# Performance work log

Measured on AMD Instinct MI355X. Metric: run time of the kernel, lower is better.

## Reference

```python
import jax, jax.numpy as jnp
import numpy as np

# Kornia's fixed 5x5 pyramid (binomial) kernel used by build_pyramid/pyrdown
_PYR_K = np.array([[1, 4, 6, 4, 1],
                   [4, 16, 24, 16, 4],
                   [6, 24, 36, 24, 6],
                   [4, 16, 24, 16, 4],
                   [1, 4, 6, 4, 1]], dtype=np.float32) / 256.0


def _pyrdown(x):
    """kornia pyrdown: 5x5 binomial blur (reflect pad) + bilinear resize to (H//2, W//2)."""
    B, C, H, W = x.shape
    xp = jnp.pad(x, ((0, 0), (0, 0), (2, 2), (2, 2)), mode='reflect')
    k = jnp.broadcast_to(jnp.asarray(_PYR_K, x.dtype), (C, 1, 5, 5))  # depthwise
    y = jax.lax.conv_general_dilated(
        xp, k, window_strides=(1, 1), padding='VALID',
        feature_group_count=C, dimension_numbers=('NCHW', 'OIHW', 'NCHW'))
    # torch F.interpolate bilinear align_corners=False == jax resize bilinear, antialias off
    return jax.image.resize(y, (B, C, H // 2, W // 2), method='bilinear', antialias=False)


def _norm_pc(x):
    """Per-channel min-max normalization to [0,1] over spatial dims."""
    mx = jnp.max(x, axis=(2, 3), keepdims=True)
    mn = jnp.min(x, axis=(2, 3), keepdims=True)
    return (x - mn) / (mx - mn)


def _avg_local_max(x):
    """Mean of 16x16 tile maxima; torch loop range(0, H-16, 16) skips the last tile
    row/col, and with zero tiles the torch code yields nan_to_num(0/0) == 0."""
    B, C, H, W = x.shape
    s = 16
    ny = len(range(0, H - s, s))
    nx = len(range(0, W - s, s))
    if ny == 0 or nx == 0:
        return jnp.zeros((B, C, 1, 1), x.dtype)
    t = x[:, :, :ny * s, :nx * s].reshape(B, C, ny, s, nx, s)
    lmax = jnp.max(t, axis=(3, 5))           # [B,C,ny,nx]
    return jnp.mean(lmax, axis=(2, 3)).reshape(B, C, 1, 1)


def _sm_normalization(x):
    d = _norm_pc(x)
    lm = _avg_local_max(d)
    return d * (1.0 - lm) ** 2


def setup_inputs() -> dict:
    key = jax.random.key(0)
    x = jax.random.normal(key, (8, 3, 512, 512), dtype=jnp.float32)
    return {"x": x}


def reference(x):
    B, C, H, W = x.shape
    inp = _norm_pc(x)
    max_level = int(H).bit_length() - 1   # 9 for H=512
    u = max_level - 1

    # Gaussian pyramid of length max_level: [inp, pyrdown(inp), ...]
    pyr = [inp]
    for _ in range(max_level - 1):
        pyr.append(_pyrdown(pyr[-1]))

    acc = None
    for i in range(u - 1):
        h, w = pyr[i + 1].shape[2], pyr[i + 1].shape[3]
        up = jnp.repeat(jnp.repeat(pyr[i + 2], 2, axis=2), 2, axis=3)[:, :, :h, :w]
        d = jnp.abs(pyr[i + 1] - up)
        nd = jax.image.resize(_sm_normalization(d), (B, C, H, W),
                              method='bilinear', antialias=False)
        acc = nd if acc is None else acc + nd

    return jnp.mean(acc, axis=1)  # [B,H,W]
```

## Files before the change

### kernel.cpp

```cpp
#include <hip/hip_runtime.h>
#include <math.h>

#define NPLANES 24
#define BLK 256
#define FINF 3.402823466e38f

__host__ __device__ __forceinline__ int d_off(int li) {
    return 2097152 - (2097152 >> (2 * li));
}

__device__ __forceinline__ int refl(int v, int S) {
    if (v < 0) v = -v;
    if (v >= S) v = 2 * S - 2 - v;
    return v;
}

__device__ __forceinline__ float bredMin(float v, float* red, int tid) {
    red[tid] = v; __syncthreads();
    for (int s = 128; s > 0; s >>= 1) {
        if (tid < s) red[tid] = fminf(red[tid], red[tid + s]);
        __syncthreads();
    }
    float r = red[0]; __syncthreads(); return r;
}
__device__ __forceinline__ float bredMax(float v, float* red, int tid) {
    red[tid] = v; __syncthreads();
    for (int s = 128; s > 0; s >>= 1) {
        if (tid < s) red[tid] = fmaxf(red[tid], red[tid + s]);
        __syncthreads();
    }
    float r = red[0]; __syncthreads(); return r;
}
__device__ __forceinline__ float bredSum(float v, float* red, int tid) {
    red[tid] = v; __syncthreads();
    for (int s = 128; s > 0; s >>= 1) {
        if (tid < s) red[tid] += red[tid + s];
        __syncthreads();
    }
    float r = red[0]; __syncthreads(); return r;
}

__device__ __forceinline__ float stencil6(const float* s, int S, int i, int j) {
    const float w[6] = {1.f, 5.f, 10.f, 10.f, 5.f, 1.f};
    int rx[6];
#pragma unroll
    for (int b = 0; b < 6; ++b) rx[b] = refl(2 * j - 2 + b, S);
    float acc = 0.f;
#pragma unroll
    for (int a = 0; a < 6; ++a) {
        int ry = refl(2 * i - 2 + a, S);
        const float* rp = s + ry * S;
        float r = 0.f;
#pragma unroll
        for (int b = 0; b < 6; ++b) r += w[b] * rp[rx[b]];
        acc += w[a] * r;
    }
    return acc * (1.f / 1024.f);
}

template <int IS, bool HAS_D, int LI>
__global__ __launch_bounds__(256) void pyrdown_tiled(const float* __restrict__ in,
                                                     float* __restrict__ out,
                                                     float* __restrict__ dout,
                                                     float* __restrict__ tileMin,
                                                     float* __restrict__ tileMax) {
    constexpr int SO = IS / 2;
    constexpr int TO = 32;
    constexpr int TI = 2 * TO + 4;
    constexpr int TPA = SO / TO;
    __shared__ float sIn[TI * TI];
    __shared__ float sH[TI * TO];
    __shared__ float sOut[TO * TO];
    __shared__ float sD[HAS_D ? 64 * 65 : 1];
    __shared__ float rmn[HAS_D ? 256 : 1], rmx[HAS_D ? 256 : 1];

    const int tid = threadIdx.x;
    const int p = blockIdx.x / (TPA * TPA);
    const int t = blockIdx.x % (TPA * TPA);
    const int ty = t / TPA, tx = t % TPA;
    const int oy = ty * TO, ox = tx * TO;
    const int iy = 2 * oy - 2, ix = 2 * ox - 2;
    const float* ip = in + (size_t)p * IS * IS;

    for (int k = tid; k < TI * TI; k += 256) {
        int r = k / TI, c = k - r * TI;
        sIn[k] = ip[refl(iy + r, IS) * IS + refl(ix + c, IS)];
    }
    __syncthreads();

    for (int k = tid; k < TI * TO; k += 256) {
        int r = k / TO, j = k - r * TO;
        const float* rp = sIn + r * TI + 2 * j;
        sH[k] = rp[0] + 5.f * rp[1] + 10.f * rp[2] + 10.f * rp[3] + 5.f * rp[4] + rp[5];
    }
    __syncthreads();

    float* op = out + (size_t)p * SO * SO;
    for (int k = tid; k < TO * TO; k += 256) {
        int i = k / TO, j = k - i * TO;
        const float* cp = sH + (2 * i) * TO + j;
        float v = (cp[0] + 5.f * cp[TO] + 10.f * cp[2 * TO] + 10.f * cp[3 * TO] +
                   5.f * cp[4 * TO] + cp[5 * TO]) * (1.f / 1024.f);
        sOut[k] = v;
        op[(size_t)(oy + i) * SO + ox + j] = v;
    }

    if (HAS_D) {
        __syncthreads();
        float* dp = dout + (size_t)p * IS * IS;
        for (int k = tid; k < 4096; k += 256) {
            int yy = k >> 6, xx = k & 63;
            float dv = fabsf(sIn[(yy + 2) * TI + xx + 2] - sOut[(yy >> 1) * TO + (xx >> 1)]);
            sD[yy * 65 + xx] = dv;
            dp[(size_t)(2 * oy + yy) * IS + 2 * ox + xx] = dv;
        }
        __syncthreads();
        int s = tid >> 4, r = tid & 15;
        int tr = s >> 2, tc = s & 3;
        const float* rowp = sD + (tr * 16 + r) * 65 + tc * 16;
        float mn = FINF, mx = -FINF;
#pragma unroll
        for (int c = 0; c < 16; ++c) {
            float v = rowp[c];
            mn = fminf(mn, v); mx = fmaxf(mx, v);
        }
        rmn[tid] = mn; rmx[tid] = mx;
        __syncthreads();
        for (int st = 8; st > 0; st >>= 1) {
            if (r < st) {
                rmn[tid] = fminf(rmn[tid], rmn[tid + st]);
                rmx[tid] = fmaxf(rmx[tid], rmx[tid + st]);
            }
            __syncthreads();
        }
        if (r == 0) {
            constexpr int TA = IS / 16;
            constexpr int baseLi = (LI == 0) ? 0 : 6144;
            int gidx = baseLi + p * TA * TA + (ty * 4 + tr) * TA + (tx * 4 + tc);
            tileMin[gidx] = rmn[tid];
            tileMax[gidx] = rmx[tid];
        }
    }
}

__global__ __launch_bounds__(256) void fused_small_kernel(const float* __restrict__ pyr3,
                                                          float* __restrict__ dBase,
                                                          float* __restrict__ A,
                                                          float* __restrict__ B) {
    __shared__ float sp3[4096], sd2[4096];
    __shared__ float sp4[1024], sd3[1024];
    __shared__ float sp5[256], sd4[256];
    __shared__ float sp6[64], sd5[64];
    __shared__ float sp7[16], sd6[16];
    __shared__ float red[256];
    __shared__ float tmaxLds[16];
    const int tid = threadIdx.x;
    const int p = blockIdx.x;
    const float* g3 = pyr3 + (size_t)p * 4096;
    for (int k = tid; k < 4096; k += 256) sp3[k] = g3[k];
    __syncthreads();

    float* d2g = dBase + d_off(2) + (size_t)p * 4096;
    for (int k = tid; k < 1024; k += 256) {
        int i = k >> 5, j = k & 31;
        float v = stencil6(sp3, 64, i, j);
        sp4[k] = v;
#pragma unroll
        for (int di = 0; di < 2; ++di)
#pragma unroll
            for (int dj = 0; dj < 2; ++dj) {
                int y = 2 * i + di, x = 2 * j + dj;
                float dv = fabsf(sp3[y * 64 + x] - v);
                sd2[y * 64 + x] = dv;
                d2g[y * 64 + x] = dv;
            }
    }
    __syncthreads();

    {
        int i = tid >> 4, j = tid & 15;
        float v = stencil6(sp4, 32, i, j);
        sp5[tid] = v;
        float* d3g = dBase + d_off(3) + (size_t)p * 1024;
#pragma unroll
        for (int di = 0; di < 2; ++di)
#pragma unroll
            for (int dj = 0; dj < 2; ++dj) {
                int y = 2 * i + di, x = 2 * j + dj;
                float dv = fabsf(sp4[y * 32 + x] - v);
                sd3[y * 32 + x] = dv;
                d3g[y * 32 + x] = dv;
            }
    }
    __syncthreads();

    if (tid < 64) {
        int i = tid >> 3, j = tid & 7;
        float v = stencil6(sp5, 16, i, j);
        sp6[tid] = v;
        float* d4g = dBase + d_off(4) + (size_t)p * 256;
#pragma unroll
        for (int di = 0; di < 2; ++di)
#pragma unroll
            for (int dj = 0; dj < 2; ++dj) {
                int y = 2 * i + di, x = 2 * j + dj;
                float dv = fabsf(sp5[y * 16 + x] - v);
                sd4[y * 16 + x] = dv;
                d4g[y * 16 + x] = dv;
            }
    }
    __syncthreads();

    if (tid < 16) {
        int i = tid >> 2, j = tid & 3;
        float v = stencil6(sp6, 8, i, j);
        sp7[tid] = v;
        float* d5g = dBase + d_off(5) + (size_t)p * 64;
#pragma unroll
        for (int di = 0; di < 2; ++di)
#pragma unroll
            for (int dj = 0; dj < 2; ++dj) {
                int y = 2 * i + di, x = 2 * j + dj;
                float dv = fabsf(sp6[y * 8 + x] - v);
                sd5[y * 8 + x] = dv;
                d5g[y * 8 + x] = dv;
            }
    }
    __syncthreads();

    if (tid < 4) {
        int i = tid >> 1, j = tid & 1;
        float v = stencil6(sp7, 4, i, j);
        float* d6g = dBase + d_off(6) + (size_t)p * 16;
#pragma unroll
        for (int di = 0; di < 2; ++di)
#pragma unroll
            for (int dj = 0; dj < 2; ++dj) {
                int y = 2 * i + di, x = 2 * j + dj;
                float dv = fabsf(sp7[y * 4 + x] - v);
                sd6[y * 4 + x] = dv;
                d6g[y * 4 + x] = dv;
            }
    }
    __syncthreads();

    {
        float mn = FINF, mx = -FINF;
        for (int k = tid; k < 4096; k += 256) {
            float v = sd2[k];
            mn = fminf(mn, v); mx = fmaxf(mx, v);
        }
        mn = bredMin(mn, red, tid);
        mx = bredMax(mx, red, tid);
        {
            int t = tid >> 4, r = tid & 15;
            int ty = t >> 2, tx = t & 3;
            const float* rowp = sd2 + (ty * 16 + r) * 64 + tx * 16;
            float sm = -FINF;
#pragma unroll
            for (int c = 0; c < 16; ++c) sm = fmaxf(sm, rowp[c]);
            red[tid] = sm;
        }
        __syncthreads();
        if (tid < 16) {
            float tm = -FINF;
            for (int r = 0; r < 16; ++r) tm = fmaxf(tm, red[tid * 16 + r]);
            tmaxLds[tid] = tm;
        }
        __syncthreads();
        if (tid == 0) {
            float s = 0.f;
            for (int ty = 0; ty < 3; ++ty)
                for (int tx = 0; tx < 3; ++tx) s += tmaxLds[ty * 4 + tx];
            float inv = 1.f / (mx - mn);
            float lm = (s * (1.f / 9.f) - mn) * inv;
            float g = (1.f - lm) * (1.f - lm);
            A[2 * NPLANES + p] = g * inv;
            B[2 * NPLANES + p] = -mn * g * inv;
        }
        __syncthreads();
    }
    {
        float mn = FINF, mx = -FINF;
        for (int k = tid; k < 1024; k += 256) {
            float v = sd3[k];
            mn = fminf(mn, v); mx = fmaxf(mx, v);
        }
        mn = bredMin(mn, red, tid);
        mx = bredMax(mx, red, tid);
        float e = sd3[(tid >> 4) * 32 + (tid & 15)];
        float tm = bredMax(e, red, tid);
        if (tid == 0) {
            float inv = 1.f / (mx - mn);
            float lm = (tm - mn) * inv;
            float g = (1.f - lm) * (1.f - lm);
            A[3 * NPLANES + p] = g * inv;
            B[3 * NPLANES + p] = -mn * g * inv;
        }
    }
    {
        float v = sd4[tid];
        float mn = bredMin(v, red, tid);
        float mx = bredMax(v, red, tid);
        if (tid == 0) {
            float inv = 1.f / (mx - mn);
            A[4 * NPLANES + p] = inv; B[4 * NPLANES + p] = -mn * inv;
        }
    }
    {
        float v = (tid < 64) ? sd5[tid] : FINF;
        float mn = bredMin(v, red, tid);
        v = (tid < 64) ? sd5[tid] : -FINF;
        float mx = bredMax(v, red, tid);
        if (tid == 0) {
            float inv = 1.f / (mx - mn);
            A[5 * NPLANES + p] = inv; B[5 * NPLANES + p] = -mn * inv;
        }
    }
    {
        float v = (tid < 16) ? sd6[tid] : FINF;
        float mn = bredMin(v, red, tid);
        v = (tid < 16) ? sd6[tid] : -FINF;
        float mx = bredMax(v, red, tid);
        if (tid == 0) {
            float inv = 1.f / (mx - mn);
            A[6 * NPLANES + p] = inv; B[6 * NPLANES + p] = -mn * inv;
        }
    }
}

__global__ __launch_bounds__(256) void reduce_kernel(const float* __restrict__ tileMin,
                                                     const float* __restrict__ tileMax,
                                                     float* __restrict__ A,
                                                     float* __restrict__ B) {
    __shared__ float red[256];
    int li = blockIdx.x / NPLANES;
    int p = blockIdx.x % NPLANES;
    int tid = threadIdx.x;
    int TP = (li == 0) ? 256 : 64;
    int TA = (li == 0) ? 16 : 8;
    int nt = TA - 1;
    int base = (li == 0) ? p * 256 : 6144 + p * 64;
    float tmn = (tid < TP) ? tileMin[base + tid] : FINF;
    float tmx = (tid < TP) ? tileMax[base + tid] : -FINF;
    float mn = bredMin(tmn, red, tid);
    float mx = bredMax(tmx, red, tid);
    int ty = (li == 0) ? (tid >> 4) : (tid >> 3);
    int tx = (li == 0) ? (tid & 15) : (tid & 7);
    float s = (tid < TP && ty < nt && tx < nt) ? tmx : 0.f;
    float sum = bredSum(s, red, tid);
    if (tid == 0) {
        float ntiles = (float)(nt * nt);
        float inv = 1.f / (mx - mn);
        float lm = (sum / ntiles - mn) * inv;
        float g = (1.f - lm) * (1.f - lm);
        A[li * NPLANES + p] = g * inv;
        B[li * NPLANES + p] = -mn * g * inv;
    }
}

__global__ __launch_bounds__(256) void final_kernel(const float* __restrict__ dBase,
                                                    const float* __restrict__ A,
                                                    const float* __restrict__ Bc,
                                                    float* __restrict__ out) {
    __shared__ float patch[1650];
    __shared__ float sBtot;
    const int tid = threadIdx.x;
    const int b = blockIdx.x >> 6;
    const int tile = blockIdx.x & 63;
    const int yb = (tile >> 3) << 6;
    const int xb = (tile & 7) << 6;

    if (tid == 0) {
        float s = 0.f;
        for (int k = 0; k < 7; ++k)
            for (int c = 0; c < 3; ++c) s += Bc[k * NPLANES + b * 3 + c];
        sBtot = s;
    }

    const int dims[7] = {34, 18, 10, 6, 4, 3, 3};
    const int lofs[7] = {0, 1156, 1480, 1580, 1616, 1632, 1641};
    int baseY[7], baseX[7];
#pragma unroll
    for (int li = 0; li < 7; ++li) {
        const int S = 256 >> li;
        const float s = 1.f / (float)(2 << li);
        baseY[li] = (int)floorf((yb + 0.5f) * s - 0.5f);
        baseX[li] = (int)floorf((xb + 0.5f) * s - 0.5f);
        const int dim = dims[li];
        const int n = dim * dim;
        const float* d0p = dBase + d_off(li) + (size_t)(b * 3) * S * S;
        const float* d1p = d0p + S * S;
        const float* d2p = d1p + S * S;
        const float A0 = A[li * NPLANES + b * 3 + 0];
        const float A1 = A[li * NPLANES + b * 3 + 1];
        const float A2 = A[li * NPLANES + b * 3 + 2];
        for (int k = tid; k < n; k += 256) {
            int r = k / dim, c = k - r * dim;
            int sr = min(max(baseY[li] + r, 0), S - 1);
            int sc = min(max(baseX[li] + c, 0), S - 1);
            int si = sr * S + sc;
            patch[lofs[li] + k] = A0 * d0p[si] + A1 * d1p[si] + A2 * d2p[si];
        }
    }
    __syncthreads();

    const int ty = tid >> 4, tx = tid & 15;
    const int gy0 = yb + (ty << 2), gx0 = xb + (tx << 2);
    float acc[4][4];
#pragma unroll
    for (int i = 0; i < 4; ++i)
#pragma unroll
        for (int j = 0; j < 4; ++j) acc[i][j] = 0.f;

#pragma unroll
    for (int li = 0; li < 7; ++li) {
        const int dim = dims[li];
        const float* P = patch + lofs[li];
        const float s = 1.f / (float)(2 << li);
        int pr[4], pc[4];
        float wy[4], wx[4];
#pragma unroll
        for (int k = 0; k < 4; ++k) {
            float fy = (gy0 + k + 0.5f) * s - 0.5f;
            float fl = floorf(fy);
            wy[k] = fy - fl;
            pr[k] = (int)fl - baseY[li];
            float fx = (gx0 + k + 0.5f) * s - 0.5f;
            fl = floorf(fx);
            wx[k] = fx - fl;
            pc[k] = (int)fl - baseX[li];
        }
#pragma unroll
        for (int i = 0; i < 4; ++i) {
            const float* r0 = P + pr[i] * dim;
            const float* r1 = r0 + dim;
#pragma unroll
            for (int j = 0; j < 4; ++j) {
                float a0 = r0[pc[j]], a1 = r0[pc[j] + 1];
                float b0 = r1[pc[j]], b1 = r1[pc[j] + 1];
                float h0 = a0 + wx[j] * (a1 - a0);
                float h1 = b0 + wx[j] * (b1 - b0);
                acc[i][j] += h0 + wy[i] * (h1 - h0);
            }
        }
    }

    const float bt = sBtot;
    float* op = out + ((size_t)b * 512 + gy0) * 512 + gx0;
#pragma unroll
    for (int i = 0; i < 4; ++i) {
        float4 v;
        v.x = (acc[i][0] + bt) * (1.f / 3.f);
        v.y = (acc[i][1] + bt) * (1.f / 3.f);
        v.z = (acc[i][2] + bt) * (1.f / 3.f);
        v.w = (acc[i][3] + bt) * (1.f / 3.f);
        *(float4*)(op + (size_t)i * 512) = v;
    }
}

extern "C" void kernel_launch(void* const* d_in, const int* in_sizes, int n_in,
                              void* d_out, int out_size, void* d_ws, size_t ws_size,
                              hipStream_t stream) {
    (void)in_sizes; (void)n_in; (void)out_size; (void)ws_size;
    const float* x = (const float*)d_in[0];
    float* ws = (float*)d_ws;
    float* out = (float*)d_out;

    float* pyr1 = ws;
    float* pyr2 = ws + 1572864;
    float* pyr3 = ws + 1966080;
    float* dBase = ws + 2064384;
    float* tileMin = ws + 4161408;
    float* tileMax = ws + 4169088;
    float* A = ws + 4176768;
    float* Bc = ws + 4176936;

    pyrdown_tiled<512, false, 0><<<NPLANES * 64, 256, 0, stream>>>(x, pyr1, nullptr, nullptr, nullptr);
    pyrdown_tiled<256, true, 0><<<NPLANES * 16, 256, 0, stream>>>(pyr1, pyr2, dBase + d_off(0), tileMin, tileMax);
    pyrdown_tiled<128, true, 1><<<NPLANES * 4, 256, 0, stream>>>(pyr2, pyr3, dBase + d_off(1), tileMin, tileMax);
    fused_small_kernel<<<NPLANES, 256, 0, stream>>>(pyr3, dBase, A, Bc);
    reduce_kernel<<<2 * NPLANES, 256, 0, stream>>>(tileMin, tileMax, A, Bc);
    final_kernel<<<8 * 64, 256, 0, stream>>>(dBase, A, Bc, out);
}
```

Before: 126.3 us.

## Fuse pyramid levels into two kernels and drop separate reduce pass

Merges the first two pyrdown levels into one tiled kernel that computes level 1 in shared memory with halo and writes only level-2 output plus d0 and tile min/max. Folds the level-2→3 pyrdown, the level-1 difference stats, and the former reduce_kernel into a per-plane monolithic kernel alongside the small-level chain. This removes the pyr1/pyr3 global round trips and three launches. In exchange it adds redundant halo recompute in the fused kernel and puts more serial work on only 24 blocks with large shared memory.

New measurement: 133.6 us. 5.7% more time.

```diff
diff --git a/kernel.cpp b/kernel.cpp
--- a/kernel.cpp
+++ b/kernel.cpp
@@ -2,7 +2,6 @@
 #include <math.h>
 
 #define NPLANES 24
-#define BLK 256
 #define FINF 3.402823466e38f
 
 __host__ __device__ __forceinline__ int d_off(int li) {
@@ -58,125 +57,227 @@
     return acc * (1.f / 1024.f);
 }
 
-template <int IS, bool HAS_D, int LI>
-__global__ __launch_bounds__(256) void pyrdown_tiled(const float* __restrict__ in,
-                                                     float* __restrict__ out,
-                                                     float* __restrict__ dout,
-                                                     float* __restrict__ tileMin,
-                                                     float* __restrict__ tileMax) {
-    constexpr int SO = IS / 2;
-    constexpr int TO = 32;
-    constexpr int TI = 2 * TO + 4;
-    constexpr int TPA = SO / TO;
-    __shared__ float sIn[TI * TI];
-    __shared__ float sH[TI * TO];
-    __shared__ float sOut[TO * TO];
-    __shared__ float sD[HAS_D ? 64 * 65 : 1];
-    __shared__ float rmn[HAS_D ? 256 : 1], rmx[HAS_D ? 256 : 1];
+__global__ __launch_bounds__(256) void fused_l12(const float* __restrict__ x,
+                                                 float* __restrict__ pyr2,
+                                                 float* __restrict__ d0,
+                                                 float* __restrict__ tileMin,
+                                                 float* __restrict__ tileMax) {
+    __shared__ float smem[18256];
+    __shared__ float red0[256], red1[256];
+    float* sX  = smem;
+    float* sH1 = smem + 10640;
+    float* sP1 = smem + 15808;
+    float* sH2 = smem;
+    float* sOut = smem + 1152;
+    float* sD  = smem + 1664;
 
     const int tid = threadIdx.x;
-    const int p = blockIdx.x / (TPA * TPA);
-    const int t = blockIdx.x % (TPA * TPA);
-    const int ty = t / TPA, tx = t % TPA;
-    const int oy = ty * TO, ox = tx * TO;
-    const int iy = 2 * oy - 2, ix = 2 * ox - 2;
-    const float* ip = in + (size_t)p * IS * IS;
-
-    for (int k = tid; k < TI * TI; k += 256) {
-        int r = k / TI, c = k - r * TI;
-        sIn[k] = ip[refl(iy + r, IS) * IS + refl(ix + c, IS)];
-    }
-    __syncthreads();
-
-    for (int k = tid; k < TI * TO; k += 256) {
-        int r = k / TO, j = k - r * TO;
-        const float* rp = sIn + r * TI + 2 * j;
-        sH[k] = rp[0] + 5.f * rp[1] + 10.f * rp[2] + 10.f * rp[3] + 5.f * rp[4] + rp[5];
-    }
-    __syncthreads();
-
-    float* op = out + (size_t)p * SO * SO;
-    for (int k = tid; k < TO * TO; k += 256) {
-        int i = k / TO, j = k - i * TO;
-        const float* cp = sH + (2 * i) * TO + j;
-        float v = (cp[0] + 5.f * cp[TO] + 10.f * cp[2 * TO] + 10.f * cp[3 * TO] +
-                   5.f * cp[4 * TO] + cp[5 * TO]) * (1.f / 1024.f);
+    const int p = blockIdx.x >> 5;
+    const int t = blockIdx.x & 31;
+    const int ty = t >> 2, tx = t & 3;
+    const int oy = ty * 16, ox = tx * 32;
+    const int p1y0 = 2 * oy - 2, p1x0 = 2 * ox - 2;
+    const int xy0 = 4 * oy - 6, xx0 = 4 * ox - 6;
+    const float* xp = x + (size_t)p * 512 * 512;
+
+    for (int k = tid; k < 76 * 140; k += 256) {
+        int r = k / 140, c = k - r * 140;
+        sX[k] = xp[refl(xy0 + r, 512) * 512 + refl(xx0 + c, 512)];
+    }
+    __syncthreads();
+    for (int k = tid; k < 76 * 68; k += 256) {
+        int r = k / 68, c1 = k - r * 68;
+        const float* rp = sX + r * 140 + 2 * c1;
+        sH1[k] = rp[0] + 5.f * rp[1] + 10.f * rp[2] + 10.f * rp[3] + 5.f * rp[4] + rp[5];
+    }
+    __syncthreads();
+    for (int k = tid; k < 36 * 68; k += 256) {
+        int r1 = k / 68, c1 = k - r1 * 68;
+        const float* cp = sH1 + 2 * r1 * 68 + c1;
+        sP1[k] = (cp[0] + 5.f * cp[68] + 10.f * cp[2 * 68] + 10.f * cp[3 * 68] +
+                  5.f * cp[4 * 68] + cp[5 * 68]) * (1.f / 1024.f);
+    }
+    __syncthreads();
+    for (int k = tid; k < 36 * 32; k += 256) {
+        int r1 = k >> 5, c2 = k & 31;
+        int b0 = 2 * (ox + c2) - 2;
+        const float* rp = sP1 + r1 * 68;
+        float s = rp[refl(b0, 256) - p1x0] + 5.f * rp[refl(b0 + 1, 256) - p1x0] +
+                  10.f * rp[refl(b0 + 2, 256) - p1x0] + 10.f * rp[refl(b0 + 3, 256) - p1x0] +
+                  5.f * rp[refl(b0 + 4, 256) - p1x0] + rp[refl(b0 + 5, 256) - p1x0];
+        sH2[k] = s;
+    }
+    __syncthreads();
+    float* o2 = pyr2 + (size_t)p * 128 * 128;
+    for (int k = tid; k < 16 * 32; k += 256) {
+        int i = k >> 5, c2 = k & 31;
+        int b0 = 2 * (oy + i) - 2;
+        float s = sH2[(refl(b0, 256) - p1y0) * 32 + c2] +
+                  5.f * sH2[(refl(b0 + 1, 256) - p1y0) * 32 + c2] +
+                  10.f * sH2[(refl(b0 + 2, 256) - p1y0) * 32 + c2] +
+                  10.f * sH2[(refl(b0 + 3, 256) - p1y0) * 32 + c2] +
+                  5.f * sH2[(refl(b0 + 4, 256) - p1y0) * 32 + c2] +
+                  sH2[(refl(b0 + 5, 256) - p1y0) * 32 + c2];
+        float v = s * (1.f / 1024.f);
         sOut[k] = v;
-        op[(size_t)(oy + i) * SO + ox + j] = v;
-    }
-
-    if (HAS_D) {
-        __syncthreads();
-        float* dp = dout + (size_t)p * IS * IS;
-        for (int k = tid; k < 4096; k += 256) {
-            int yy = k >> 6, xx = k & 63;
-            float dv = fabsf(sIn[(yy + 2) * TI + xx + 2] - sOut[(yy >> 1) * TO + (xx >> 1)]);
-            sD[yy * 65 + xx] = dv;
-            dp[(size_t)(2 * oy + yy) * IS + 2 * ox + xx] = dv;
-        }
-        __syncthreads();
-        int s = tid >> 4, r = tid & 15;
-        int tr = s >> 2, tc = s & 3;
-        const float* rowp = sD + (tr * 16 + r) * 65 + tc * 16;
+        o2[(size_t)(oy + i) * 128 + ox + c2] = v;
+    }
+    __syncthreads();
+    float* dp = d0 + (size_t)p * 256 * 256;
+    for (int k = tid; k < 32 * 64; k += 256) {
+        int yy = k >> 6, xx = k & 63;
+        float dv = fabsf(sP1[(yy + 2) * 68 + xx + 2] - sOut[(yy >> 1) * 32 + (xx >> 1)]);
+        sD[yy * 65 + xx] = dv;
+        dp[(size_t)(2 * oy + yy) * 256 + 2 * ox + xx] = dv;
+    }
+    __syncthreads();
+    {
+        int s8 = tid >> 5, l = tid & 31;
+        int tr = s8 >> 2, tc = s8 & 3;
+        int rr = l >> 1, ch = (l & 1) * 8;
+        const float* rowp = sD + (tr * 16 + rr) * 65 + tc * 16 + ch;
         float mn = FINF, mx = -FINF;
 #pragma unroll
-        for (int c = 0; c < 16; ++c) {
+        for (int c = 0; c < 8; ++c) {
             float v = rowp[c];
             mn = fminf(mn, v); mx = fmaxf(mx, v);
         }
-        rmn[tid] = mn; rmx[tid] = mx;
-        __syncthreads();
-        for (int st = 8; st > 0; st >>= 1) {
-            if (r < st) {
-                rmn[tid] = fminf(rmn[tid], rmn[tid + st]);
-                rmx[tid] = fmaxf(rmx[tid], rmx[tid + st]);
+        red0[tid] = mn; red1[tid] = mx;
+        __syncthreads();
+        for (int st = 16; st > 0; st >>= 1) {
+            if (l < st) {
+                red0[tid] = fminf(red0[tid], red0[tid + st]);
+                red1[tid] = fmaxf(red1[tid], red1[tid + st]);
             }
             __syncthreads();
         }
-        if (r == 0) {
-            constexpr int TA = IS / 16;
-            constexpr int baseLi = (LI == 0) ? 0 : 6144;
-            int gidx = baseLi + p * TA * TA + (ty * 4 + tr) * TA + (tx * 4 + tc);
-            tileMin[gidx] = rmn[tid];
-            tileMax[gidx] = rmx[tid];
-        }
-    }
-}
-
-__global__ __launch_bounds__(256) void fused_small_kernel(const float* __restrict__ pyr3,
-                                                          float* __restrict__ dBase,
-                                                          float* __restrict__ A,
-                                                          float* __restrict__ B) {
-    __shared__ float sp3[4096], sd2[4096];
-    __shared__ float sp4[1024], sd3[1024];
-    __shared__ float sp5[256], sd4[256];
-    __shared__ float sp6[64], sd5[64];
-    __shared__ float sp7[16], sd6[16];
+        if (l == 0) {
+            int gidx = p * 256 + (2 * ty + tr) * 16 + (4 * tx + tc);
+            tileMin[gidx] = red0[tid];
+            tileMax[gidx] = red1[tid];
+        }
+    }
+}
+
+__global__ __launch_bounds__(256) void plane_monolith(const float* __restrict__ pyr2,
+                                                      float* __restrict__ dBase,
+                                                      const float* __restrict__ tileMin,
+                                                      const float* __restrict__ tileMax,
+                                                      float* __restrict__ A,
+                                                      float* __restrict__ B) {
+    __shared__ float smem[28672];
     __shared__ float red[256];
-    __shared__ float tmaxLds[16];
+    __shared__ float tMn[64], tMx[64], tmaxLds[16];
+    float* sP2 = smem;
+    float* sH  = smem + 16384;
+    float* sP3 = smem + 24576;
+    float* sd2 = sH;
+    float* sp4 = sH + 4096;
+    float* sd3 = sH + 5120;
+    float* sp5 = sH + 6144;
+    float* sd4 = sH + 6400;
+    float* sp6 = sH + 6656;
+    float* sd5 = sH + 6720;
+    float* sp7 = sH + 6784;
+    float* sd6 = sH + 6800;
     const int tid = threadIdx.x;
     const int p = blockIdx.x;
-    const float* g3 = pyr3 + (size_t)p * 4096;
-    for (int k = tid; k < 4096; k += 256) sp3[k] = g3[k];
+
+    const float4* gp = (const float4*)(pyr2 + (size_t)p * 16384);
+    float4* sv = (float4*)sP2;
+    for (int k = tid; k < 4096; k += 256) sv[k] = gp[k];
+    __syncthreads();
+    for (int k = tid; k < 8192; k += 256) {
+        int r = k >> 6, c = k & 63;
+        int b0 = 2 * c - 2;
+        const float* rp = sP2 + r * 128;
+        sH[k] = rp[refl(b0, 128)] + 5.f * rp[refl(b0 + 1, 128)] + 10.f * rp[refl(b0 + 2, 128)] +
+                10.f * rp[refl(b0 + 3, 128)] + 5.f * rp[refl(b0 + 4, 128)] + rp[refl(b0 + 5, 128)];
+    }
+    __syncthreads();
+    for (int k = tid; k < 4096; k += 256) {
+        int r3 = k >> 6, c = k & 63;
+        int b0 = 2 * r3 - 2;
+        float s = sH[refl(b0, 128) * 64 + c] + 5.f * sH[refl(b0 + 1, 128) * 64 + c] +
+                  10.f * sH[refl(b0 + 2, 128) * 64 + c] + 10.f * sH[refl(b0 + 3, 128) * 64 + c] +
+                  5.f * sH[refl(b0 + 4, 128) * 64 + c] + sH[refl(b0 + 5, 128) * 64 + c];
+        sP3[k] = s * (1.f / 1024.f);
+    }
+    __syncthreads();
+    float* d1g = dBase + d_off(1) + (size_t)p * 16384;
+    for (int k = tid; k < 16384; k += 256) {
+        int y = k >> 7, xc = k & 127;
+        float dv = fabsf(sP2[k] - sP3[(y >> 1) * 64 + (xc >> 1)]);
+        sP2[k] = dv;
+        d1g[k] = dv;
+    }
+    __syncthreads();
+    {
+        int s = tid >> 2, q = tid & 3;
+        int tr = s >> 3, tc = s & 7;
+        float mn = FINF, mx = -FINF;
+        for (int r = 0; r < 16; ++r) {
+            const float* pp = sP2 + (tr * 16 + r) * 128 + tc * 16 + q * 4;
+#pragma unroll
+            for (int j = 0; j < 4; ++j) {
+                float v = pp[j];
+                mn = fminf(mn, v); mx = fmaxf(mx, v);
+            }
+        }
+        __shared__ float r0[256], r1[256];
+        r0[tid] = mn; r1[tid] = mx;
+        __syncthreads();
+        if (q < 2) { r0[tid] = fminf(r0[tid], r0[tid + 2]); r1[tid] = fmaxf(r1[tid], r1[tid + 2]); }
+        __syncthreads();
+        if (q == 0) { tMn[s] = fminf(r0[tid], r0[tid + 1]); tMx[s] = fmaxf(r1[tid], r1[tid + 1]); }
+        __syncthreads();
+        float a = (tid < 64) ? tMn[tid] : FINF;
+        float b = (tid < 64) ? tMx[tid] : -FINF;
+        float mnp = bredMin(a, red, tid);
+        float mxp = bredMax(b, red, tid);
+        float su = (tid < 64 && (tid >> 3) < 7 && (tid & 7) < 7) ? tMx[tid] : 0.f;
+        float sum = bredSum(su, red, tid);
+        if (tid == 0) {
+            float inv = 1.f / (mxp - mnp);
+            float lm = (sum * (1.f / 49.f) - mnp) * inv;
+            float g = (1.f - lm) * (1.f - lm);
+            A[1 * NPLANES + p] = g * inv;
+            B[1 * NPLANES + p] = -mnp * g * inv;
+        }
+    }
+    {
+        float tmn = tileMin[p * 256 + tid];
+        float tmx = tileMax[p * 256 + tid];
+        float mnp = bredMin(tmn, red, tid);
+        float mxp = bredMax(tmx, red, tid);
+        float su = ((tid >> 4) < 15 && (tid & 15) < 15) ? tmx : 0.f;
+        float sum = bredSum(su, red, tid);
+        if (tid == 0) {
+            float inv = 1.f / (mxp - mnp);
+            float lm = (sum * (1.f / 225.f) - mnp) * inv;
+            float g = (1.f - lm) * (1.f - lm);
+            A[0 * NPLANES + p] = g * inv;
+            B[0 * NPLANES + p] = -mnp * g * inv;
+        }
+    }
     __syncthreads();
 
     float* d2g = dBase + d_off(2) + (size_t)p * 4096;
     for (int k = tid; k < 1024; k += 256) {
         int i = k >> 5, j = k & 31;
-        float v = stencil6(sp3, 64, i, j);
+        float v = stencil6(sP3, 64, i, j);
         sp4[k] = v;
 #pragma unroll
         for (int di = 0; di < 2; ++di)
 #pragma unroll
             for (int dj = 0; dj < 2; ++dj) {
-                int y = 2 * i + di, x = 2 * j + dj;
-                float dv = fabsf(sp3[y * 64 + x] - v);
-                sd2[y * 64 + x] = dv;
-                d2g[y * 64 + x] = dv;
-            }
-    }
-    __syncthreads();
-
+                int y = 2 * i + di, xx = 2 * j + dj;
+                float dv = fabsf(sP3[y * 64 + xx] - v);
+                sd2[y * 64 + xx] = dv;
+                d2g[y * 64 + xx] = dv;
+            }
+    }
+    __syncthreads();
     {
         int i = tid >> 4, j = tid & 15;
         float v = stencil6(sp4, 32, i, j);
@@ -186,14 +287,13 @@
         for (int di = 0; di < 2; ++di)
 #pragma unroll
             for (int dj = 0; dj < 2; ++dj) {
-                int y = 2 * i + di, x = 2 * j + dj;
-                float dv = fabsf(sp4[y * 32 + x] - v);
-                sd3[y * 32 + x] = dv;
-                d3g[y * 32 + x] = dv;
-            }
-    }
-    __syncthreads();
-
+                int y = 2 * i + di, xx = 2 * j + dj;
+                float dv = fabsf(sp4[y * 32 + xx] - v);
+                sd3[y * 32 + xx] = dv;
+                d3g[y * 32 + xx] = dv;
+            }
+    }
+    __syncthreads();
     if (tid < 64) {
         int i = tid >> 3, j = tid & 7;
         float v = stencil6(sp5, 16, i, j);
@@ -203,14 +303,13 @@
         for (int di = 0; di < 2; ++di)
 #pragma unroll
             for (int dj = 0; dj < 2; ++dj) {
-                int y = 2 * i + di, x = 2 * j + dj;
-                float dv = fabsf(sp5[y * 16 + x] - v);
-                sd4[y * 16 + x] = dv;
-                d4g[y * 16 + x] = dv;
-            }
-    }
-    __syncthreads();
-
+                int y = 2 * i + di, xx = 2 * j + dj;
+                float dv = fabsf(sp5[y * 16 + xx] - v);
+                sd4[y * 16 + xx] = dv;
+                d4g[y * 16 + xx] = dv;
+            }
+    }
+    __syncthreads();
     if (tid < 16) {
         int i = tid >> 2, j = tid & 3;
         float v = stencil6(sp6, 8, i, j);
@@ -220,14 +319,13 @@
         for (int di = 0; di < 2; ++di)
 #pragma unroll
             for (int dj = 0; dj < 2; ++dj) {
-                int y = 2 * i + di, x = 2 * j + dj;
-                float dv = fabsf(sp6[y * 8 + x] - v);
-                sd5[y * 8 + x] = dv;
-                d5g[y * 8 + x] = dv;
-            }
-    }
-    __syncthreads();
-
+                int y = 2 * i + di, xx = 2 * j + dj;
+                float dv = fabsf(sp6[y * 8 + xx] - v);
+                sd5[y * 8 + xx] = dv;
+                d5g[y * 8 + xx] = dv;
+            }
+    }
+    __syncthreads();
     if (tid < 4) {
         int i = tid >> 1, j = tid & 1;
         float v = stencil6(sp7, 4, i, j);
@@ -236,10 +334,10 @@
         for (int di = 0; di < 2; ++di)
 #pragma unroll
             for (int dj = 0; dj < 2; ++dj) {
-                int y = 2 * i + di, x = 2 * j + dj;
-                float dv = fabsf(sp7[y * 4 + x] - v);
-                sd6[y * 4 + x] = dv;
-                d6g[y * 4 + x] = dv;
+                int y = 2 * i + di, xx = 2 * j + dj;
+                float dv = fabsf(sp7[y * 4 + xx] - v);
+                sd6[y * 4 + xx] = dv;
+                d6g[y * 4 + xx] = dv;
             }
     }
     __syncthreads();
@@ -326,36 +424,6 @@
             float inv = 1.f / (mx - mn);
             A[6 * NPLANES + p] = inv; B[6 * NPLANES + p] = -mn * inv;
         }
-    }
-}
-
-__global__ __launch_bounds__(256) void reduce_kernel(const float* __restrict__ tileMin,
-                                                     const float* __restrict__ tileMax,
-                                                     float* __restrict__ A,
-                                                     float* __restrict__ B) {
-    __shared__ float red[256];
-    int li = blockIdx.x / NPLANES;
-    int p = blockIdx.x % NPLANES;
-    int tid = threadIdx.x;
-    int TP = (li == 0) ? 256 : 64;
-    int TA = (li == 0) ? 16 : 8;
-    int nt = TA - 1;
-    int base = (li == 0) ? p * 256 : 6144 + p * 64;
-    float tmn = (tid < TP) ? tileMin[base + tid] : FINF;
-    float tmx = (tid < TP) ? tileMax[base + tid] : -FINF;
-    float mn = bredMin(tmn, red, tid);
-    float mx = bredMax(tmx, red, tid);
-    int ty = (li == 0) ? (tid >> 4) : (tid >> 3);
-    int tx = (li == 0) ? (tid & 15) : (tid & 7);
-    float s = (tid < TP && ty < nt && tx < nt) ? tmx : 0.f;
-    float sum = bredSum(s, red, tid);
-    if (tid == 0) {
-        float ntiles = (float)(nt * nt);
-        float inv = 1.f / (mx - mn);
-        float lm = (sum / ntiles - mn) * inv;
-        float g = (1.f - lm) * (1.f - lm);
-        A[li * NPLANES + p] = g * inv;
-        B[li * NPLANES + p] = -mn * g * inv;
     }
 }
 
@@ -467,19 +535,14 @@
     float* ws = (float*)d_ws;
     float* out = (float*)d_out;
 
-    float* pyr1 = ws;
-    float* pyr2 = ws + 1572864;
-    float* pyr3 = ws + 1966080;
-    float* dBase = ws + 2064384;
-    float* tileMin = ws + 4161408;
-    float* tileMax = ws + 4169088;
-    float* A = ws + 4176768;
-    float* Bc = ws + 4176936;
-
-    pyrdown_tiled<512, false, 0><<<NPLANES * 64, 256, 0, stream>>>(x, pyr1, nullptr, nullptr, nullptr);
-    pyrdown_tiled<256, true, 0><<<NPLANES * 16, 256, 0, stream>>>(pyr1, pyr2, dBase + d_off(0), tileMin, tileMax);
-    pyrdown_tiled<128, true, 1><<<NPLANES * 4, 256, 0, stream>>>(pyr2, pyr3, dBase + d_off(1), tileMin, tileMax);
-    fused_small_kernel<<<NPLANES, 256, 0, stream>>>(pyr3, dBase, A, Bc);
-    reduce_kernel<<<2 * NPLANES, 256, 0, stream>>>(tileMin, tileMax, A, Bc);
+    float* pyr2 = ws;
+    float* dBase = ws + 393216;
+    float* tileMin = ws + 2490240;
+    float* tileMax = ws + 2496384;
+    float* A = ws + 2502528;
+    float* Bc = ws + 2502696;
+
+    fused_l12<<<NPLANES * 32, 256, 0, stream>>>(x, pyr2, dBase + d_off(0), tileMin, tileMax);
+    plane_monolith<<<NPLANES, 256, 0, stream>>>(pyr2, dBase, tileMin, tileMax, A, Bc);
     final_kernel<<<8 * 64, 256, 0, stream>>>(dBase, A, Bc, out);
 }
```

## Fold reduce kernel into fused small kernel with 1024 threads and shuffle reductions

Applied to the files above, without the earlier changes.

Removes the separate reduce_kernel launch by computing the level-0/1 normalization coefficients inside fused_small_kernel, which now runs with 1024 threads per block. LDS tree reductions are replaced with wavefront shuffle reductions plus a small cross-wave step. The final kernel's bilinear upsampling loads a small register patch once per level instead of doing four LDS reads per output pixel. The 1024-thread block raises register pressure and leaves many threads idle in the small-level stages.

Result: faster. 119.3 us (-5.5%).

```diff
diff --git a/kernel.cpp b/kernel.cpp
--- a/kernel.cpp
+++ b/kernel.cpp
@@ -2,7 +2,6 @@
 #include <math.h>
 
 #define NPLANES 24
-#define BLK 256
 #define FINF 3.402823466e38f
 
 __host__ __device__ __forceinline__ int d_off(int li) {
@@ -15,29 +14,65 @@
     return v;
 }
 
-__device__ __forceinline__ float bredMin(float v, float* red, int tid) {
-    red[tid] = v; __syncthreads();
-    for (int s = 128; s > 0; s >>= 1) {
-        if (tid < s) red[tid] = fminf(red[tid], red[tid + s]);
-        __syncthreads();
-    }
-    float r = red[0]; __syncthreads(); return r;
-}
-__device__ __forceinline__ float bredMax(float v, float* red, int tid) {
-    red[tid] = v; __syncthreads();
-    for (int s = 128; s > 0; s >>= 1) {
-        if (tid < s) red[tid] = fmaxf(red[tid], red[tid + s]);
-        __syncthreads();
-    }
-    float r = red[0]; __syncthreads(); return r;
-}
-__device__ __forceinline__ float bredSum(float v, float* red, int tid) {
-    red[tid] = v; __syncthreads();
-    for (int s = 128; s > 0; s >>= 1) {
-        if (tid < s) red[tid] += red[tid + s];
-        __syncthreads();
-    }
-    float r = red[0]; __syncthreads(); return r;
+__device__ __forceinline__ float wmin64(float v) {
+#pragma unroll
+    for (int o = 32; o > 0; o >>= 1) v = fminf(v, __shfl_down(v, o, 64));
+    return v;
+}
+__device__ __forceinline__ float wmax64(float v) {
+#pragma unroll
+    for (int o = 32; o > 0; o >>= 1) v = fmaxf(v, __shfl_down(v, o, 64));
+    return v;
+}
+__device__ __forceinline__ float wsum64(float v) {
+#pragma unroll
+    for (int o = 32; o > 0; o >>= 1) v += __shfl_down(v, o, 64);
+    return v;
+}
+__device__ __forceinline__ float bmin1024(float v, float* cross, int tid) {
+    v = wmin64(v);
+    if ((tid & 63) == 0) cross[tid >> 6] = v;
+    __syncthreads();
+    if (tid < 16) {
+        float t = cross[tid];
+#pragma unroll
+        for (int o = 8; o > 0; o >>= 1) t = fminf(t, __shfl_down(t, o, 16));
+        if (tid == 0) cross[0] = t;
+    }
+    __syncthreads();
+    float r = cross[0];
+    __syncthreads();
+    return r;
+}
+__device__ __forceinline__ float bmax1024(float v, float* cross, int tid) {
+    v = wmax64(v);
+    if ((tid & 63) == 0) cross[tid >> 6] = v;
+    __syncthreads();
+    if (tid < 16) {
+        float t = cross[tid];
+#pragma unroll
+        for (int o = 8; o > 0; o >>= 1) t = fmaxf(t, __shfl_down(t, o, 16));
+        if (tid == 0) cross[0] = t;
+    }
+    __syncthreads();
+    float r = cross[0];
+    __syncthreads();
+    return r;
+}
+__device__ __forceinline__ float bsum1024(float v, float* cross, int tid) {
+    v = wsum64(v);
+    if ((tid & 63) == 0) cross[tid >> 6] = v;
+    __syncthreads();
+    if (tid < 16) {
+        float t = cross[tid];
+#pragma unroll
+        for (int o = 8; o > 0; o >>= 1) t += __shfl_down(t, o, 16);
+        if (tid == 0) cross[0] = t;
+    }
+    __syncthreads();
+    float r = cross[0];
+    __syncthreads();
+    return r;
 }
 
 __device__ __forceinline__ float stencil6(const float* s, int S, int i, int j) {
@@ -143,28 +178,31 @@
     }
 }
 
-__global__ __launch_bounds__(256) void fused_small_kernel(const float* __restrict__ pyr3,
-                                                          float* __restrict__ dBase,
-                                                          float* __restrict__ A,
-                                                          float* __restrict__ B) {
+__global__ __launch_bounds__(1024) void fused_small_kernel(const float* __restrict__ pyr3,
+                                                           float* __restrict__ dBase,
+                                                           const float* __restrict__ tileMin,
+                                                           const float* __restrict__ tileMax,
+                                                           float* __restrict__ A,
+                                                           float* __restrict__ B) {
     __shared__ float sp3[4096], sd2[4096];
     __shared__ float sp4[1024], sd3[1024];
     __shared__ float sp5[256], sd4[256];
     __shared__ float sp6[64], sd5[64];
     __shared__ float sp7[16], sd6[16];
-    __shared__ float red[256];
+    __shared__ float cross[16];
+    __shared__ float strip[256];
     __shared__ float tmaxLds[16];
     const int tid = threadIdx.x;
     const int p = blockIdx.x;
-    const float* g3 = pyr3 + (size_t)p * 4096;
-    for (int k = tid; k < 4096; k += 256) sp3[k] = g3[k];
-    __syncthreads();
-
-    float* d2g = dBase + d_off(2) + (size_t)p * 4096;
-    for (int k = tid; k < 1024; k += 256) {
-        int i = k >> 5, j = k & 31;
+
+    ((float4*)sp3)[tid] = ((const float4*)(pyr3 + (size_t)p * 4096))[tid];
+    __syncthreads();
+
+    {
+        float* d2g = dBase + d_off(2) + (size_t)p * 4096;
+        int i = tid >> 5, j = tid & 31;
         float v = stencil6(sp3, 64, i, j);
-        sp4[k] = v;
+        sp4[tid] = v;
 #pragma unroll
         for (int di = 0; di < 2; ++di)
 #pragma unroll
@@ -176,8 +214,7 @@
             }
     }
     __syncthreads();
-
-    {
+    if (tid < 256) {
         int i = tid >> 4, j = tid & 15;
         float v = stencil6(sp4, 32, i, j);
         sp5[tid] = v;
@@ -193,7 +230,6 @@
             }
     }
     __syncthreads();
-
     if (tid < 64) {
         int i = tid >> 3, j = tid & 7;
         float v = stencil6(sp5, 16, i, j);
@@ -210,7 +246,6 @@
             }
     }
     __syncthreads();
-
     if (tid < 16) {
         int i = tid >> 2, j = tid & 3;
         float v = stencil6(sp6, 8, i, j);
@@ -227,7 +262,6 @@
             }
     }
     __syncthreads();
-
     if (tid < 4) {
         int i = tid >> 1, j = tid & 1;
         float v = stencil6(sp7, 4, i, j);
@@ -245,26 +279,24 @@
     __syncthreads();
 
     {
-        float mn = FINF, mx = -FINF;
-        for (int k = tid; k < 4096; k += 256) {
-            float v = sd2[k];
-            mn = fminf(mn, v); mx = fmaxf(mx, v);
-        }
-        mn = bredMin(mn, red, tid);
-        mx = bredMax(mx, red, tid);
-        {
+        float4 q = ((const float4*)sd2)[tid];
+        float mn = fminf(fminf(q.x, q.y), fminf(q.z, q.w));
+        float mx = fmaxf(fmaxf(q.x, q.y), fmaxf(q.z, q.w));
+        mn = bmin1024(mn, cross, tid);
+        mx = bmax1024(mx, cross, tid);
+        if (tid < 256) {
             int t = tid >> 4, r = tid & 15;
             int ty = t >> 2, tx = t & 3;
             const float* rowp = sd2 + (ty * 16 + r) * 64 + tx * 16;
             float sm = -FINF;
 #pragma unroll
             for (int c = 0; c < 16; ++c) sm = fmaxf(sm, rowp[c]);
-            red[tid] = sm;
+            strip[tid] = sm;
         }
         __syncthreads();
         if (tid < 16) {
             float tm = -FINF;
-            for (int r = 0; r < 16; ++r) tm = fmaxf(tm, red[tid * 16 + r]);
+            for (int r = 0; r < 16; ++r) tm = fmaxf(tm, strip[tid * 16 + r]);
             tmaxLds[tid] = tm;
         }
         __syncthreads();
@@ -281,15 +313,11 @@
         __syncthreads();
     }
     {
-        float mn = FINF, mx = -FINF;
-        for (int k = tid; k < 1024; k += 256) {
-            float v = sd3[k];
-            mn = fminf(mn, v); mx = fmaxf(mx, v);
-        }
-        mn = bredMin(mn, red, tid);
-        mx = bredMax(mx, red, tid);
-        float e = sd3[(tid >> 4) * 32 + (tid & 15)];
-        float tm = bredMax(e, red, tid);
+        float v = sd3[tid];
+        float mn = bmin1024(v, cross, tid);
+        float mx = bmax1024(v, cross, tid);
+        float e = (tid < 256) ? sd3[(tid >> 4) * 32 + (tid & 15)] : -FINF;
+        float tm = bmax1024(e, cross, tid);
         if (tid == 0) {
             float inv = 1.f / (mx - mn);
             float lm = (tm - mn) * inv;
@@ -299,9 +327,10 @@
         }
     }
     {
-        float v = sd4[tid];
-        float mn = bredMin(v, red, tid);
-        float mx = bredMax(v, red, tid);
+        float v = (tid < 256) ? sd4[tid] : FINF;
+        float mn = bmin1024(v, cross, tid);
+        v = (tid < 256) ? sd4[tid] : -FINF;
+        float mx = bmax1024(v, cross, tid);
         if (tid == 0) {
             float inv = 1.f / (mx - mn);
             A[4 * NPLANES + p] = inv; B[4 * NPLANES + p] = -mn * inv;
@@ -309,9 +338,9 @@
     }
     {
         float v = (tid < 64) ? sd5[tid] : FINF;
-        float mn = bredMin(v, red, tid);
+        float mn = bmin1024(v, cross, tid);
         v = (tid < 64) ? sd5[tid] : -FINF;
-        float mx = bredMax(v, red, tid);
+        float mx = bmax1024(v, cross, tid);
         if (tid == 0) {
             float inv = 1.f / (mx - mn);
             A[5 * NPLANES + p] = inv; B[5 * NPLANES + p] = -mn * inv;
@@ -319,43 +348,43 @@
     }
     {
         float v = (tid < 16) ? sd6[tid] : FINF;
-        float mn = bredMin(v, red, tid);
+        float mn = bmin1024(v, cross, tid);
         v = (tid < 16) ? sd6[tid] : -FINF;
-        float mx = bredMax(v, red, tid);
+        float mx = bmax1024(v, cross, tid);
         if (tid == 0) {
             float inv = 1.f / (mx - mn);
             A[6 * NPLANES + p] = inv; B[6 * NPLANES + p] = -mn * inv;
         }
     }
-}
-
-__global__ __launch_bounds__(256) void reduce_kernel(const float* __restrict__ tileMin,
-                                                     const float* __restrict__ tileMax,
-                                                     float* __restrict__ A,
-                                                     float* __restrict__ B) {
-    __shared__ float red[256];
-    int li = blockIdx.x / NPLANES;
-    int p = blockIdx.x % NPLANES;
-    int tid = threadIdx.x;
-    int TP = (li == 0) ? 256 : 64;
-    int TA = (li == 0) ? 16 : 8;
-    int nt = TA - 1;
-    int base = (li == 0) ? p * 256 : 6144 + p * 64;
-    float tmn = (tid < TP) ? tileMin[base + tid] : FINF;
-    float tmx = (tid < TP) ? tileMax[base + tid] : -FINF;
-    float mn = bredMin(tmn, red, tid);
-    float mx = bredMax(tmx, red, tid);
-    int ty = (li == 0) ? (tid >> 4) : (tid >> 3);
-    int tx = (li == 0) ? (tid & 15) : (tid & 7);
-    float s = (tid < TP && ty < nt && tx < nt) ? tmx : 0.f;
-    float sum = bredSum(s, red, tid);
-    if (tid == 0) {
-        float ntiles = (float)(nt * nt);
-        float inv = 1.f / (mx - mn);
-        float lm = (sum / ntiles - mn) * inv;
-        float g = (1.f - lm) * (1.f - lm);
-        A[li * NPLANES + p] = g * inv;
-        B[li * NPLANES + p] = -mn * g * inv;
+    {
+        float tmn = (tid < 256) ? tileMin[p * 256 + tid] : FINF;
+        float tmx = (tid < 256) ? tileMax[p * 256 + tid] : -FINF;
+        float mn = bmin1024(tmn, cross, tid);
+        float mx = bmax1024(tmx, cross, tid);
+        float su = (tid < 256 && (tid >> 4) < 15 && (tid & 15) < 15) ? tmx : 0.f;
+        float sum = bsum1024(su, cross, tid);
+        if (tid == 0) {
+            float inv = 1.f / (mx - mn);
+            float lm = (sum * (1.f / 225.f) - mn) * inv;
+            float g = (1.f - lm) * (1.f - lm);
+            A[0 * NPLANES + p] = g * inv;
+            B[0 * NPLANES + p] = -mn * g * inv;
+        }
+    }
+    {
+        float tmn = (tid < 64) ? tileMin[6144 + p * 64 + tid] : FINF;
+        float tmx = (tid < 64) ? tileMax[6144 + p * 64 + tid] : -FINF;
+        float mn = bmin1024(tmn, cross, tid);
+        float mx = bmax1024(tmx, cross, tid);
+        float su = (tid < 64 && (tid >> 3) < 7 && (tid & 7) < 7) ? tmx : 0.f;
+        float sum = bsum1024(su, cross, tid);
+        if (tid == 0) {
+            float inv = 1.f / (mx - mn);
+            float lm = (sum * (1.f / 49.f) - mn) * inv;
+            float g = (1.f - lm) * (1.f - lm);
+            A[1 * NPLANES + p] = g * inv;
+            B[1 * NPLANES + p] = -mn * g * inv;
+        }
     }
 }
 
@@ -363,7 +392,7 @@
                                                     const float* __restrict__ A,
                                                     const float* __restrict__ Bc,
                                                     float* __restrict__ out) {
-    __shared__ float patch[1650];
+    __shared__ float patch[1700];
     __shared__ float sBtot;
     const int tid = threadIdx.x;
     const int b = blockIdx.x >> 6;
@@ -413,34 +442,89 @@
 #pragma unroll
         for (int j = 0; j < 4; ++j) acc[i][j] = 0.f;
 
-#pragma unroll
-    for (int li = 0; li < 7; ++li) {
+    {
+        const int dim = 34;
+        float wy[4], wx[4];
+        int ry[4], cx[4];
+#pragma unroll
+        for (int k = 0; k < 4; ++k) {
+            float fy = (gy0 + k + 0.5f) * 0.5f - 0.5f;
+            float fl = floorf(fy);
+            wy[k] = fy - fl; ry[k] = (int)fl - baseY[0];
+            float fx = (gx0 + k + 0.5f) * 0.5f - 0.5f;
+            fl = floorf(fx);
+            wx[k] = fx - fl; cx[k] = (int)fl - baseX[0];
+        }
+        const int r0 = ry[0], c0 = cx[0];
+        const float* pp = patch + r0 * dim + c0;
+        float P[4][4];
+#pragma unroll
+        for (int r = 0; r < 4; ++r)
+#pragma unroll
+            for (int c = 0; c < 4; ++c) P[r][c] = pp[r * dim + c];
+        float h[4][4];
+#pragma unroll
+        for (int j = 0; j < 4; ++j) {
+            int dx = cx[j] - c0;
+#pragma unroll
+            for (int r = 0; r < 4; ++r) {
+                float a = dx == 0 ? P[r][0] : (dx == 1 ? P[r][1] : P[r][2]);
+                float bb = dx == 0 ? P[r][1] : (dx == 1 ? P[r][2] : P[r][3]);
+                h[r][j] = a + wx[j] * (bb - a);
+            }
+        }
+#pragma unroll
+        for (int i = 0; i < 4; ++i) {
+            int dy = ry[i] - r0;
+#pragma unroll
+            for (int j = 0; j < 4; ++j) {
+                float h0 = dy == 0 ? h[0][j] : (dy == 1 ? h[1][j] : h[2][j]);
+                float h1 = dy == 0 ? h[1][j] : (dy == 1 ? h[2][j] : h[3][j]);
+                acc[i][j] += h0 + wy[i] * (h1 - h0);
+            }
+        }
+    }
+#pragma unroll
+    for (int li = 1; li < 7; ++li) {
         const int dim = dims[li];
-        const float* P = patch + lofs[li];
+        const float* P0 = patch + lofs[li];
         const float s = 1.f / (float)(2 << li);
-        int pr[4], pc[4];
         float wy[4], wx[4];
+        int ry[4], cx[4];
 #pragma unroll
         for (int k = 0; k < 4; ++k) {
             float fy = (gy0 + k + 0.5f) * s - 0.5f;
             float fl = floorf(fy);
-            wy[k] = fy - fl;
-            pr[k] = (int)fl - baseY[li];
+            wy[k] = fy - fl; ry[k] = (int)fl - baseY[li];
             float fx = (gx0 + k + 0.5f) * s - 0.5f;
             fl = floorf(fx);
-            wx[k] = fx - fl;
-            pc[k] = (int)fl - baseX[li];
+            wx[k] = fx - fl; cx[k] = (int)fl - baseX[li];
+        }
+        const int r0 = ry[0], c0 = cx[0];
+        const float* pp = P0 + r0 * dim + c0;
+        float P[3][3];
+#pragma unroll
+        for (int r = 0; r < 3; ++r)
+#pragma unroll
+            for (int c = 0; c < 3; ++c) P[r][c] = pp[r * dim + c];
+        float h[3][4];
+#pragma unroll
+        for (int j = 0; j < 4; ++j) {
+            int dx = cx[j] - c0;
+#pragma unroll
+            for (int r = 0; r < 3; ++r) {
+                float a = dx == 0 ? P[r][0] : P[r][1];
+                float bb = dx == 0 ? P[r][1] : P[r][2];
+                h[r][j] = a + wx[j] * (bb - a);
+            }
         }
 #pragma unroll
         for (int i = 0; i < 4; ++i) {
-            const float* r0 = P + pr[i] * dim;
-            const float* r1 = r0 + dim;
+            int dy = ry[i] - r0;
 #pragma unroll
             for (int j = 0; j < 4; ++j) {
-                float a0 = r0[pc[j]], a1 = r0[pc[j] + 1];
-                float b0 = r1[pc[j]], b1 = r1[pc[j] + 1];
-                float h0 = a0 + wx[j] * (a1 - a0);
-                float h1 = b0 + wx[j] * (b1 - b0);
+                float h0 = dy == 0 ? h[0][j] : h[1][j];
+                float h1 = dy == 0 ? h[1][j] : h[2][j];
                 acc[i][j] += h0 + wy[i] * (h1 - h0);
             }
         }
@@ -479,7 +563,6 @@
     pyrdown_tiled<512, false, 0><<<NPLANES * 64, 256, 0, stream>>>(x, pyr1, nullptr, nullptr, nullptr);
     pyrdown_tiled<256, true, 0><<<NPLANES * 16, 256, 0, stream>>>(pyr1, pyr2, dBase + d_off(0), tileMin, tileMax);
     pyrdown_tiled<128, true, 1><<<NPLANES * 4, 256, 0, stream>>>(pyr2, pyr3, dBase + d_off(1), tileMin, tileMax);
-    fused_small_kernel<<<NPLANES, 256, 0, stream>>>(pyr3, dBase, A, Bc);
-    reduce_kernel<<<2 * NPLANES, 256, 0, stream>>>(tileMin, tileMax, A, Bc);
+    fused_small_kernel<<<NPLANES, 1024, 0, stream>>>(pyr3, dBase, tileMin, tileMax, A, Bc);
     final_kernel<<<8 * 64, 256, 0, stream>>>(dBase, A, Bc, out);
 }
```
